# Kernel optimization log

Hardware: AMD Instinct MI355X
Metric: run time of the kernel (lower is better)

Reference implementation:

```python
import jax, jax.numpy as jnp
import numpy as np

RADIUS2 = 0.03 ** 2
SIM_THRESH = 0.7
EPS = 1e-8


def setup_inputs() -> dict:
    key = jax.random.key(0)
    k1, k2, k3, k4, k5, k6, k7 = jax.random.split(key, 7)
    B, N, D = 2, 6144, 32
    # points in a 0.3-side cube so radius 0.03 gives realistic neighbor counts
    points = jax.random.uniform(k1, (B, N, 3), dtype=jnp.float32) * 0.3
    embeddings = jax.random.normal(k2, (B, N, D), dtype=jnp.float32)
    leaf_mask = jax.random.randint(k3, (B, N), 0, 2, dtype=jnp.int32)
    # consistency_net: Linear(2D, D) -> ReLU -> Linear(D, D)
    W1 = jax.random.normal(k4, (2 * D, D), dtype=jnp.float32) * (1.0 / np.sqrt(2 * D))
    b1 = jax.random.normal(k5, (D,), dtype=jnp.float32) * 0.01
    W2 = jax.random.normal(k6, (D, D), dtype=jnp.float32) * (1.0 / np.sqrt(D))
    b2 = jax.random.normal(k7, (D,), dtype=jnp.float32) * 0.01
    return {"points": points, "embeddings": embeddings, "leaf_mask": leaf_mask,
            "W1": W1, "b1": b1, "W2": W2, "b2": b2}


def reference(points, embeddings, leaf_mask, W1, b1, W2, b2):
    # points: [B,N,3], embeddings: [B,N,D], leaf_mask: [B,N] int (0/1)
    dt = embeddings.dtype
    leaf = leaf_mask > 0  # [B,N] bool

    # pairwise squared distances via the Gram trick (avoids [B,N,N,3])
    pn = jnp.sum(points * points, axis=-1)                      # [B,N]
    gram = jnp.einsum('bic,bjc->bij', points, points)           # [B,N,N]
    d2 = jnp.maximum(pn[:, :, None] + pn[:, None, :] - 2.0 * gram, 0.0)

    # neighbor mask: within radius AND neighbor is leaf (matches dist<0.03 & leaf_mask)
    nb = (d2 < RADIUS2) & leaf[:, None, :]                      # [B,N,N]

    # cosine similarity with torch's eps clamp on norms
    enorm = jnp.maximum(jnp.linalg.norm(embeddings, axis=-1), EPS)  # [B,N]
    inner = jnp.einsum('bid,bjd->bij', embeddings, embeddings)      # [B,N,N]
    sims = inner / (enorm[:, :, None] * enorm[:, None, :])

    sim_mask = nb & (sims > SIM_THRESH)                          # [B,N,N]
    cnt_nb = jnp.sum(nb, axis=-1)                                # [B,N]
    cnt_sim = jnp.sum(sim_mask, axis=-1)                         # [B,N]

    # mean of similar-neighbor embeddings
    sum_sim = jnp.einsum('bij,bjd->bid', sim_mask.astype(dt), embeddings)
    mean_sim = sum_sim / jnp.maximum(cnt_sim, 1).astype(dt)[..., None]

    # consistency MLP on [center_embedding, mean_similar]
    combined = jnp.concatenate([embeddings, mean_sim], axis=-1)  # [B,N,2D]
    h = jax.nn.relu(jnp.einsum('bnk,kd->bnd', combined, W1) + b1)
    out = jnp.einsum('bnk,kd->bnd', h, W2) + b2                  # [B,N,D]

    # refine only leaf points with >1 neighbor and >0 similar neighbors
    cond = leaf & (cnt_nb > 1) & (cnt_sim > 0)                   # [B,N]
    refined = jnp.where(cond[..., None], out, embeddings)

    # per-batch early exit: sum(leaf_mask) < 10 -> unchanged
    batch_ok = jnp.sum(leaf_mask, axis=-1) >= 10                 # [B]
    return jnp.where(batch_ok[:, None, None], refined, embeddings)
```

## Files before the change

### kernel.cpp

```cpp
#include <hip/hip_runtime.h>

#define NPTS    6144
#define DIM     32
#define NB      2
#define NCELL   1000
#define R2      0.0009f
#define NWAVES  4
#define BLOCK   (NWAVES * 64)
#define LEAFBIT 8192
#define PPT     6
#define NBCAP   128
#define COPYBLK 64

__device__ __forceinline__ int cellof(float x) {
    int c = (int)(x * (10.0f / 0.3f));
    return min(max(c, 0), 9);
}

#define WS_LEAF   0
#define WS_CSTART 4
#define WS_SORTED 2008

__global__ __launch_bounds__(1024)
void build_cells(const float* __restrict__ points, const int* __restrict__ leaf,
                 const float* __restrict__ emb, float* __restrict__ out,
                 int* __restrict__ ws)
{
    __shared__ int s_hist[1024];
    __shared__ int s_cursor[1024];
    __shared__ int s_wsum[16];
    __shared__ int s_leaf;

    if (blockIdx.x >= NB) {
        const int cb = blockIdx.x - NB;
        const float4* src = (const float4*)emb;
        float4*       dst = (float4*)out;
        const int total = NB * NPTS * (DIM / 4);
        for (int i = cb * 1024 + threadIdx.x; i < total; i += COPYBLK * 1024)
            dst[i] = src[i];
        return;
    }

    const int t = threadIdx.x;
    const int b = blockIdx.x;
    const int w = t >> 6, lane = t & 63;

    s_hist[t] = 0;
    if (t == 0) s_leaf = 0;

    float px[PPT], py[PPT], pz[PPT];
    int   pc[PPT], pw[PPT];

    __syncthreads();

    int lc = 0;
    #pragma unroll
    for (int r = 0; r < PPT; ++r) {
        const int i  = r * 1024 + t;
        const int gi = b * NPTS + i;
        px[r] = points[gi * 3 + 0];
        py[r] = points[gi * 3 + 1];
        pz[r] = points[gi * 3 + 2];
        const int lf = leaf[gi] > 0 ? 1 : 0;
        lc += lf;
        pc[r] = (cellof(pz[r]) * 10 + cellof(py[r])) * 10 + cellof(px[r]);
        pw[r] = i + (lf ? LEAFBIT : 0);
        atomicAdd(&s_hist[pc[r]], 1);
    }
    #pragma unroll
    for (int off = 32; off > 0; off >>= 1) lc += __shfl_down(lc, off);
    if (lane == 0) atomicAdd(&s_leaf, lc);
    __syncthreads();

    const int v = s_hist[t];
    int x = v;
    #pragma unroll
    for (int off = 1; off < 64; off <<= 1) {
        const int y = __shfl_up(x, off);
        if (lane >= off) x += y;
    }
    if (lane == 63) s_wsum[w] = x;
    __syncthreads();
    if (t < 16) {
        int wv = s_wsum[t];
        #pragma unroll
        for (int off = 1; off < 16; off <<= 1) {
            const int y = __shfl_up(wv, off);
            if (t >= off) wv += y;
        }
        s_wsum[t] = wv;
    }
    __syncthreads();
    const int incl = x + (w > 0 ? s_wsum[w - 1] : 0);
    s_cursor[t] = incl - v;

    if (t < NCELL) ws[WS_CSTART + b * (NCELL + 1) + t + 1] = incl;
    if (t == 0) {
        ws[WS_CSTART + b * (NCELL + 1)] = 0;
        ws[WS_LEAF + b] = s_leaf;
    }
    __syncthreads();

    float4* sorted = (float4*)(ws + WS_SORTED) + (size_t)b * NPTS;
    #pragma unroll
    for (int r = 0; r < PPT; ++r) {
        const int pos = atomicAdd(&s_cursor[pc[r]], 1);
        sorted[pos] = make_float4(px[r], py[r], pz[r], (float)pw[r]);
    }
}

__global__ __launch_bounds__(BLOCK)
void refine(const float* __restrict__ emb,
            const float* __restrict__ W1, const float* __restrict__ b1,
            const float* __restrict__ W2, const float* __restrict__ b2,
            const int* __restrict__ ws, float* __restrict__ out)
{
    __shared__ __align__(16) float s_ei[NWAVES][DIM];
    __shared__ float s_mean[NWAVES][DIM];
    __shared__ float s_h[NWAVES][DIM];
    __shared__ int   s_nb[NWAVES][NBCAP];
    __shared__ int   s_sv[NWAVES][NBCAP];

    const int tid  = threadIdx.x;
    const int wid  = tid >> 6;
    const int lane = tid & 63;
    const int s    = blockIdx.x * NWAVES + wid;
    const int b    = s / NPTS;
    const int slot = s - b * NPTS;

    if (ws[WS_LEAF + b] < 10) return;

    const float4* srt  = (const float4*)(ws + WS_SORTED) + (size_t)b * NPTS;
    const int*    cst  = ws + WS_CSTART + b * (NCELL + 1);
    const float*  embB = emb + (size_t)b * NPTS * DIM;

    const float4 P  = srt[slot];
    const int    iw = (int)P.w;
    if (!(iw & LEAFBIT)) return;
    const int io = iw & (LEAFBIT - 1);

    const float* ei = embB + (size_t)io * DIM;
    float ev = 0.0f;
    if (lane < DIM) { ev = ei[lane]; s_ei[wid][lane] = ev; }
    float nsq = ev * ev;
    #pragma unroll
    for (int off = 16; off > 0; off >>= 1) nsq += __shfl_xor(nsq, off);
    const float ni2 = __shfl(nsq, 0);
    const float rni = 1.0f / fmaxf(sqrtf(ni2), 1e-8f);

    const int cx = cellof(P.x), cy = cellof(P.y), cz = cellof(P.z);

    int begv = 0, lenv = 0;
    if (lane < 9) {
        const int z = cz + lane / 3 - 1;
        const int y = cy + lane % 3 - 1;
        if ((unsigned)z <= 9u && (unsigned)y <= 9u) {
            const int rowb = (z * 10 + y) * 10;
            const int c0   = rowb + max(cx - 1, 0);
            const int c1   = rowb + min(cx + 1, 9);
            begv = cst[c0];
            lenv = cst[c1 + 1] - begv;
        }
    }
    const int rb0 = __shfl(begv, 0), rb1 = __shfl(begv, 1), rb2 = __shfl(begv, 2);
    const int rb3 = __shfl(begv, 3), rb4 = __shfl(begv, 4), rb5 = __shfl(begv, 5);
    const int rb6 = __shfl(begv, 6), rb7 = __shfl(begv, 7), rb8 = __shfl(begv, 8);
    const int ln0 = __shfl(lenv, 0), ln1 = __shfl(lenv, 1), ln2 = __shfl(lenv, 2);
    const int ln3 = __shfl(lenv, 3), ln4 = __shfl(lenv, 4), ln5 = __shfl(lenv, 5);
    const int ln6 = __shfl(lenv, 6), ln7 = __shfl(lenv, 7), ln8 = __shfl(lenv, 8);
    const int pf1 = ln0,       pf2 = pf1 + ln1, pf3 = pf2 + ln2;
    const int pf4 = pf3 + ln3, pf5 = pf4 + ln4, pf6 = pf5 + ln5;
    const int pf7 = pf6 + ln6, pf8 = pf7 + ln7, pf9 = pf8 + ln8;

    int nbcnt = 0;
    for (int base = 0; base < pf9; base += 64) {
        const int g = base + lane;
        int j = 0;
        if (g < pf9) j = rb8 + g - pf8;
        if (g < pf8) j = rb7 + g - pf7;
        if (g < pf7) j = rb6 + g - pf6;
        if (g < pf6) j = rb5 + g - pf5;
        if (g < pf5) j = rb4 + g - pf4;
        if (g < pf4) j = rb3 + g - pf3;
        if (g < pf3) j = rb2 + g - pf2;
        if (g < pf2) j = rb1 + g - pf1;
        if (g < pf1) j = rb0 + g;
        const float4 Q  = srt[j];
        const float dx = Q.x - P.x, dy = Q.y - P.y, dz = Q.z - P.z;
        const float d2 = dx * dx + dy * dy + dz * dz;
        const int   jw = (int)Q.w;
        const bool  nb = (g < pf9) && (d2 < R2) && ((jw & LEAFBIT) != 0);
        const unsigned long long m = __ballot(nb);
        if (nb) {
            const int pos = nbcnt + __popcll(m & ((1ull << lane) - 1ull));
            if (pos < NBCAP) s_nb[wid][pos] = jw & (LEAFBIT - 1);
        }
        nbcnt += __popcll(m);
    }
    const int cnt_nb = nbcnt;

    const int d    = lane & 31;
    const int half = lane >> 5;
    int csim = 0;
    const int nh = min(cnt_nb, NBCAP);
    for (int h0 = 0; h0 < nh; h0 += 32) {
        const int h = h0 + d;
        float dot = 0.0f, nj2 = 0.0f;
        int   jo  = 0;
        if (h < nh) {
            jo = s_nb[wid][h];
            const float4* ej4 = (const float4*)(embB + (size_t)jo * DIM) + half * 4;
            #pragma unroll
            for (int k = 0; k < 4; ++k) {
                const float4 v = ej4[k];
                const float4 a = *(const float4*)&s_ei[wid][16 * half + 4 * k];
                dot += a.x * v.x + a.y * v.y + a.z * v.z + a.w * v.w;
                nj2 += v.x * v.x + v.y * v.y + v.z * v.z + v.w * v.w;
            }
        }
        dot += __shfl_xor(dot, 32);
        nj2 += __shfl_xor(nj2, 32);
        bool surv = false;
        if (h < nh && half == 0) {
            const float rnj = 1.0f / fmaxf(sqrtf(nj2), 1e-8f);
            surv = (dot * rni * rnj) > 0.7f;
        }
        const unsigned long long m = __ballot(surv);
        if (surv) {
            const int pos = csim + __popcll(m & ((1ull << lane) - 1ull));
            s_sv[wid][pos] = jo;
        }
        csim += __popcll(m);
    }

    if (!((cnt_nb > 1) && (csim > 0))) return;

    float msum = 0.0f;
    for (int v = half; v < csim; v += 2)
        msum += embB[(size_t)s_sv[wid][v] * DIM + d];
    msum += __shfl_xor(msum, 32);
    if (half == 0) s_mean[wid][d] = msum / (float)csim;

    float a = (half == 0) ? b1[d] : 0.0f;
    #pragma unroll
    for (int k = 0; k < 16; ++k) {
        const int kk = half * 16 + k;
        a = fmaf(s_ei[wid][kk], W1[kk * DIM + d], a);
    }
    #pragma unroll
    for (int k = 0; k < 16; ++k) {
        const int kk = half * 16 + k;
        a = fmaf(s_mean[wid][kk], W1[(DIM + kk) * DIM + d], a);
    }
    a += __shfl_xor(a, 32);
    if (half == 0) s_h[wid][d] = fmaxf(a, 0.0f);

    float c = (half == 0) ? b2[d] : 0.0f;
    #pragma unroll
    for (int k = 0; k < 16; ++k) {
        const int kk = half * 16 + k;
        c = fmaf(s_h[wid][kk], W2[kk * DIM + d], c);
    }
    c += __shfl_xor(c, 32);
    if (half == 0)
        out[((size_t)b * NPTS + io) * DIM + d] = c;
}

extern "C" void kernel_launch(void* const* d_in, const int* in_sizes, int n_in,
                              void* d_out, int out_size, void* d_ws, size_t ws_size,
                              hipStream_t stream) {
    const float* points = (const float*)d_in[0];
    const float* emb    = (const float*)d_in[1];
    const int*   leaf   = (const int*)d_in[2];
    const float* W1     = (const float*)d_in[3];
    const float* b1     = (const float*)d_in[4];
    const float* W2     = (const float*)d_in[5];
    const float* b2     = (const float*)d_in[6];
    float*       outp   = (float*)d_out;
    int*         ws     = (int*)d_ws;

    build_cells<<<NB + COPYBLK, 1024, 0, stream>>>(points, leaf, emb, outp, ws);

    const int grid = (NB * NPTS) / NWAVES;
    refine<<<grid, BLOCK, 0, stream>>>(emb, W1, b1, W2, b2, ws, outp);
}
```

Measured before the change: 86.85 us.

## Fuse cell build and refine into one kernel with per-block redundant grid in LDS

Merges the cell-sorting kernel and the refine kernel into a single launch. Each of 256 blocks redundantly rebuilds its batch's sorted point grid and cell starts in shared memory (about 130KB), then each wave processes a contiguous run of points and writes either the copied embedding or the MLP output. This removes the second launch, the global workspace round trip and the separate bulk copy. In exchange, every block repeats the full histogram and sort work and uses a large LDS footprint, which limits occupancy to one block per CU.

```diff
diff --git a/kernel.cpp b/kernel.cpp
--- a/kernel.cpp
+++ b/kernel.cpp
@@ -5,48 +5,59 @@
 #define NB      2
 #define NCELL   1000
 #define R2      0.0009f
-#define NWAVES  4
-#define BLOCK   (NWAVES * 64)
 #define LEAFBIT 8192
 #define PPT     6
 #define NBCAP   128
-#define COPYBLK 64
+#define CHUNKS  128
+#define SPB     (NPTS / CHUNKS)
+#define WPB     16
+#define SPW     (SPB / WPB)
+
+#define SM_PTS    0
+#define SM_CST    98304
+#define SM_HIST   102400
+#define SM_CUR    106496
+#define SM_WSUM   110592
+#define SM_LEAF   110656
+#define SM_NB     110720
+#define SM_SV     118912
+#define SM_EI     127104
+#define SM_MEAN   129152
+#define SM_H      131200
+#define SMEM_BYTES 133248
 
 __device__ __forceinline__ int cellof(float x) {
     int c = (int)(x * (10.0f / 0.3f));
     return min(max(c, 0), 9);
 }
 
-#define WS_LEAF   0
-#define WS_CSTART 4
-#define WS_SORTED 2008
-
 __global__ __launch_bounds__(1024)
-void build_cells(const float* __restrict__ points, const int* __restrict__ leaf,
-                 const float* __restrict__ emb, float* __restrict__ out,
-                 int* __restrict__ ws)
+void fused(const float* __restrict__ points, const int* __restrict__ leaf,
+           const float* __restrict__ emb,
+           const float* __restrict__ W1, const float* __restrict__ b1,
+           const float* __restrict__ W2, const float* __restrict__ b2,
+           float* __restrict__ out)
 {
-    __shared__ int s_hist[1024];
-    __shared__ int s_cursor[1024];
-    __shared__ int s_wsum[16];
-    __shared__ int s_leaf;
-
-    if (blockIdx.x >= NB) {
-        const int cb = blockIdx.x - NB;
-        const float4* src = (const float4*)emb;
-        float4*       dst = (float4*)out;
-        const int total = NB * NPTS * (DIM / 4);
-        for (int i = cb * 1024 + threadIdx.x; i < total; i += COPYBLK * 1024)
-            dst[i] = src[i];
-        return;
-    }
-
-    const int t = threadIdx.x;
-    const int b = blockIdx.x;
-    const int w = t >> 6, lane = t & 63;
+    extern __shared__ char smem[];
+    float4* s_pts   = (float4*)(smem + SM_PTS);
+    int*    s_cst   = (int*)(smem + SM_CST);
+    int*    s_hist  = (int*)(smem + SM_HIST);
+    int*    s_cur   = (int*)(smem + SM_CUR);
+    int*    s_wsum  = (int*)(smem + SM_WSUM);
+    int*    s_leafp = (int*)(smem + SM_LEAF);
+    int*    s_nb    = (int*)(smem + SM_NB);
+    int*    s_sv    = (int*)(smem + SM_SV);
+    float*  s_ei    = (float*)(smem + SM_EI);
+    float*  s_mean  = (float*)(smem + SM_MEAN);
+    float*  s_h     = (float*)(smem + SM_H);
+
+    const int t     = threadIdx.x;
+    const int b     = blockIdx.x / CHUNKS;
+    const int chunk = blockIdx.x - b * CHUNKS;
+    const int wid   = t >> 6, lane = t & 63;
 
     s_hist[t] = 0;
-    if (t == 0) s_leaf = 0;
+    if (t == 0) *s_leafp = 0;
 
     float px[PPT], py[PPT], pz[PPT];
     int   pc[PPT], pw[PPT];
@@ -69,7 +80,7 @@
     }
     #pragma unroll
     for (int off = 32; off > 0; off >>= 1) lc += __shfl_down(lc, off);
-    if (lane == 0) atomicAdd(&s_leaf, lc);
+    if (lane == 0) atomicAdd(s_leafp, lc);
     __syncthreads();
 
     const int v = s_hist[t];
@@ -79,7 +90,7 @@
         const int y = __shfl_up(x, off);
         if (lane >= off) x += y;
     }
-    if (lane == 63) s_wsum[w] = x;
+    if (lane == 63) s_wsum[wid] = x;
     __syncthreads();
     if (t < 16) {
         int wv = s_wsum[t];
@@ -91,184 +102,173 @@
         s_wsum[t] = wv;
     }
     __syncthreads();
-    const int incl = x + (w > 0 ? s_wsum[w - 1] : 0);
-    s_cursor[t] = incl - v;
-
-    if (t < NCELL) ws[WS_CSTART + b * (NCELL + 1) + t + 1] = incl;
-    if (t == 0) {
-        ws[WS_CSTART + b * (NCELL + 1)] = 0;
-        ws[WS_LEAF + b] = s_leaf;
-    }
-    __syncthreads();
-
-    float4* sorted = (float4*)(ws + WS_SORTED) + (size_t)b * NPTS;
+    const int incl = x + (wid > 0 ? s_wsum[wid - 1] : 0);
+    s_cur[t] = incl - v;
+    if (t < NCELL) s_cst[t + 1] = incl;
+    if (t == 0) s_cst[0] = 0;
+    __syncthreads();
+
     #pragma unroll
     for (int r = 0; r < PPT; ++r) {
-        const int pos = atomicAdd(&s_cursor[pc[r]], 1);
-        sorted[pos] = make_float4(px[r], py[r], pz[r], (float)pw[r]);
-    }
-}
-
-__global__ __launch_bounds__(BLOCK)
-void refine(const float* __restrict__ emb,
-            const float* __restrict__ W1, const float* __restrict__ b1,
-            const float* __restrict__ W2, const float* __restrict__ b2,
-            const int* __restrict__ ws, float* __restrict__ out)
-{
-    __shared__ __align__(16) float s_ei[NWAVES][DIM];
-    __shared__ float s_mean[NWAVES][DIM];
-    __shared__ float s_h[NWAVES][DIM];
-    __shared__ int   s_nb[NWAVES][NBCAP];
-    __shared__ int   s_sv[NWAVES][NBCAP];
-
-    const int tid  = threadIdx.x;
-    const int wid  = tid >> 6;
-    const int lane = tid & 63;
-    const int s    = blockIdx.x * NWAVES + wid;
-    const int b    = s / NPTS;
-    const int slot = s - b * NPTS;
-
-    if (ws[WS_LEAF + b] < 10) return;
-
-    const float4* srt  = (const float4*)(ws + WS_SORTED) + (size_t)b * NPTS;
-    const int*    cst  = ws + WS_CSTART + b * (NCELL + 1);
-    const float*  embB = emb + (size_t)b * NPTS * DIM;
-
-    const float4 P  = srt[slot];
-    const int    iw = (int)P.w;
-    if (!(iw & LEAFBIT)) return;
-    const int io = iw & (LEAFBIT - 1);
-
-    const float* ei = embB + (size_t)io * DIM;
-    float ev = 0.0f;
-    if (lane < DIM) { ev = ei[lane]; s_ei[wid][lane] = ev; }
-    float nsq = ev * ev;
-    #pragma unroll
-    for (int off = 16; off > 0; off >>= 1) nsq += __shfl_xor(nsq, off);
-    const float ni2 = __shfl(nsq, 0);
-    const float rni = 1.0f / fmaxf(sqrtf(ni2), 1e-8f);
-
-    const int cx = cellof(P.x), cy = cellof(P.y), cz = cellof(P.z);
-
-    int begv = 0, lenv = 0;
-    if (lane < 9) {
-        const int z = cz + lane / 3 - 1;
-        const int y = cy + lane % 3 - 1;
-        if ((unsigned)z <= 9u && (unsigned)y <= 9u) {
-            const int rowb = (z * 10 + y) * 10;
-            const int c0   = rowb + max(cx - 1, 0);
-            const int c1   = rowb + min(cx + 1, 9);
-            begv = cst[c0];
-            lenv = cst[c1 + 1] - begv;
-        }
-    }
-    const int rb0 = __shfl(begv, 0), rb1 = __shfl(begv, 1), rb2 = __shfl(begv, 2);
-    const int rb3 = __shfl(begv, 3), rb4 = __shfl(begv, 4), rb5 = __shfl(begv, 5);
-    const int rb6 = __shfl(begv, 6), rb7 = __shfl(begv, 7), rb8 = __shfl(begv, 8);
-    const int ln0 = __shfl(lenv, 0), ln1 = __shfl(lenv, 1), ln2 = __shfl(lenv, 2);
-    const int ln3 = __shfl(lenv, 3), ln4 = __shfl(lenv, 4), ln5 = __shfl(lenv, 5);
-    const int ln6 = __shfl(lenv, 6), ln7 = __shfl(lenv, 7), ln8 = __shfl(lenv, 8);
-    const int pf1 = ln0,       pf2 = pf1 + ln1, pf3 = pf2 + ln2;
-    const int pf4 = pf3 + ln3, pf5 = pf4 + ln4, pf6 = pf5 + ln5;
-    const int pf7 = pf6 + ln6, pf8 = pf7 + ln7, pf9 = pf8 + ln8;
-
-    int nbcnt = 0;
-    for (int base = 0; base < pf9; base += 64) {
-        const int g = base + lane;
-        int j = 0;
-        if (g < pf9) j = rb8 + g - pf8;
-        if (g < pf8) j = rb7 + g - pf7;
-        if (g < pf7) j = rb6 + g - pf6;
-        if (g < pf6) j = rb5 + g - pf5;
-        if (g < pf5) j = rb4 + g - pf4;
-        if (g < pf4) j = rb3 + g - pf3;
-        if (g < pf3) j = rb2 + g - pf2;
-        if (g < pf2) j = rb1 + g - pf1;
-        if (g < pf1) j = rb0 + g;
-        const float4 Q  = srt[j];
-        const float dx = Q.x - P.x, dy = Q.y - P.y, dz = Q.z - P.z;
-        const float d2 = dx * dx + dy * dy + dz * dz;
-        const int   jw = (int)Q.w;
-        const bool  nb = (g < pf9) && (d2 < R2) && ((jw & LEAFBIT) != 0);
-        const unsigned long long m = __ballot(nb);
-        if (nb) {
-            const int pos = nbcnt + __popcll(m & ((1ull << lane) - 1ull));
-            if (pos < NBCAP) s_nb[wid][pos] = jw & (LEAFBIT - 1);
-        }
-        nbcnt += __popcll(m);
-    }
-    const int cnt_nb = nbcnt;
-
-    const int d    = lane & 31;
-    const int half = lane >> 5;
-    int csim = 0;
-    const int nh = min(cnt_nb, NBCAP);
-    for (int h0 = 0; h0 < nh; h0 += 32) {
-        const int h = h0 + d;
-        float dot = 0.0f, nj2 = 0.0f;
-        int   jo  = 0;
-        if (h < nh) {
-            jo = s_nb[wid][h];
-            const float4* ej4 = (const float4*)(embB + (size_t)jo * DIM) + half * 4;
-            #pragma unroll
-            for (int k = 0; k < 4; ++k) {
-                const float4 v = ej4[k];
-                const float4 a = *(const float4*)&s_ei[wid][16 * half + 4 * k];
-                dot += a.x * v.x + a.y * v.y + a.z * v.z + a.w * v.w;
-                nj2 += v.x * v.x + v.y * v.y + v.z * v.z + v.w * v.w;
-            }
-        }
-        dot += __shfl_xor(dot, 32);
-        nj2 += __shfl_xor(nj2, 32);
-        bool surv = false;
-        if (h < nh && half == 0) {
-            const float rnj = 1.0f / fmaxf(sqrtf(nj2), 1e-8f);
-            surv = (dot * rni * rnj) > 0.7f;
-        }
-        const unsigned long long m = __ballot(surv);
-        if (surv) {
-            const int pos = csim + __popcll(m & ((1ull << lane) - 1ull));
-            s_sv[wid][pos] = jo;
-        }
-        csim += __popcll(m);
-    }
-
-    if (!((cnt_nb > 1) && (csim > 0))) return;
-
-    float msum = 0.0f;
-    for (int v = half; v < csim; v += 2)
-        msum += embB[(size_t)s_sv[wid][v] * DIM + d];
-    msum += __shfl_xor(msum, 32);
-    if (half == 0) s_mean[wid][d] = msum / (float)csim;
-
-    float a = (half == 0) ? b1[d] : 0.0f;
-    #pragma unroll
-    for (int k = 0; k < 16; ++k) {
-        const int kk = half * 16 + k;
-        a = fmaf(s_ei[wid][kk], W1[kk * DIM + d], a);
-    }
-    #pragma unroll
-    for (int k = 0; k < 16; ++k) {
-        const int kk = half * 16 + k;
-        a = fmaf(s_mean[wid][kk], W1[(DIM + kk) * DIM + d], a);
-    }
-    a += __shfl_xor(a, 32);
-    if (half == 0) s_h[wid][d] = fmaxf(a, 0.0f);
-
-    float c = (half == 0) ? b2[d] : 0.0f;
-    #pragma unroll
-    for (int k = 0; k < 16; ++k) {
-        const int kk = half * 16 + k;
-        c = fmaf(s_h[wid][kk], W2[kk * DIM + d], c);
-    }
-    c += __shfl_xor(c, 32);
-    if (half == 0)
-        out[((size_t)b * NPTS + io) * DIM + d] = c;
+        const int pos = atomicAdd(&s_cur[pc[r]], 1);
+        s_pts[pos] = make_float4(px[r], py[r], pz[r], (float)pw[r]);
+    }
+    __syncthreads();
+
+    const bool   ok   = *s_leafp >= 10;
+    const float* embB = emb + (size_t)b * NPTS * DIM;
+    float*       outB = out + (size_t)b * NPTS * DIM;
+    const int    dd   = lane & 31;
+    const int    half = lane >> 5;
+
+    for (int rs = 0; rs < SPW; ++rs) {
+        const int io = chunk * SPB + wid * SPW + rs;
+        const int gi = b * NPTS + io;
+        const float Px = points[gi * 3 + 0];
+        const float Py = points[gi * 3 + 1];
+        const float Pz = points[gi * 3 + 2];
+        const bool  li = leaf[gi] > 0;
+
+        const float4* e4   = (const float4*)(embB + (size_t)io * DIM);
+        float4*       out4 = (float4*)(outB + (size_t)io * DIM);
+
+        if (!(ok && li)) {
+            if (lane < DIM / 4) out4[lane] = e4[lane];
+            continue;
+        }
+
+        float ev = 0.0f;
+        if (lane < DIM) { ev = ((const float*)e4)[lane]; s_ei[wid * DIM + lane] = ev; }
+        float nsq = ev * ev;
+        #pragma unroll
+        for (int off = 16; off > 0; off >>= 1) nsq += __shfl_xor(nsq, off);
+        const float ni2 = __shfl(nsq, 0);
+        const float rni = 1.0f / fmaxf(sqrtf(ni2), 1e-8f);
+
+        const int cx = cellof(Px), cy = cellof(Py), cz = cellof(Pz);
+
+        int begv = 0, lenv = 0;
+        if (lane < 9) {
+            const int z = cz + lane / 3 - 1;
+            const int y = cy + lane % 3 - 1;
+            if ((unsigned)z <= 9u && (unsigned)y <= 9u) {
+                const int rowb = (z * 10 + y) * 10;
+                const int c0   = rowb + max(cx - 1, 0);
+                const int c1   = rowb + min(cx + 1, 9);
+                begv = s_cst[c0];
+                lenv = s_cst[c1 + 1] - begv;
+            }
+        }
+        const int rb0 = __shfl(begv, 0), rb1 = __shfl(begv, 1), rb2 = __shfl(begv, 2);
+        const int rb3 = __shfl(begv, 3), rb4 = __shfl(begv, 4), rb5 = __shfl(begv, 5);
+        const int rb6 = __shfl(begv, 6), rb7 = __shfl(begv, 7), rb8 = __shfl(begv, 8);
+        const int ln0 = __shfl(lenv, 0), ln1 = __shfl(lenv, 1), ln2 = __shfl(lenv, 2);
+        const int ln3 = __shfl(lenv, 3), ln4 = __shfl(lenv, 4), ln5 = __shfl(lenv, 5);
+        const int ln6 = __shfl(lenv, 6), ln7 = __shfl(lenv, 7), ln8 = __shfl(lenv, 8);
+        const int pf1 = ln0,       pf2 = pf1 + ln1, pf3 = pf2 + ln2;
+        const int pf4 = pf3 + ln3, pf5 = pf4 + ln4, pf6 = pf5 + ln5;
+        const int pf7 = pf6 + ln6, pf8 = pf7 + ln7, pf9 = pf8 + ln8;
+
+        int nbcnt = 0;
+        for (int base = 0; base < pf9; base += 64) {
+            const int g = base + lane;
+            int j = 0;
+            if (g < pf9) j = rb8 + g - pf8;
+            if (g < pf8) j = rb7 + g - pf7;
+            if (g < pf7) j = rb6 + g - pf6;
+            if (g < pf6) j = rb5 + g - pf5;
+            if (g < pf5) j = rb4 + g - pf4;
+            if (g < pf4) j = rb3 + g - pf3;
+            if (g < pf3) j = rb2 + g - pf2;
+            if (g < pf2) j = rb1 + g - pf1;
+            if (g < pf1) j = rb0 + g;
+            const float4 Q  = s_pts[j];
+            const float dx = Q.x - Px, dy = Q.y - Py, dz = Q.z - Pz;
+            const float d2 = dx * dx + dy * dy + dz * dz;
+            const int   jw = (int)Q.w;
+            const bool  nb = (g < pf9) && (d2 < R2) && ((jw & LEAFBIT) != 0);
+            const unsigned long long m = __ballot(nb);
+            if (nb) {
+                const int pos = nbcnt + __popcll(m & ((1ull << lane) - 1ull));
+                if (pos < NBCAP) s_nb[wid * NBCAP + pos] = jw & (LEAFBIT - 1);
+            }
+            nbcnt += __popcll(m);
+        }
+        const int cnt_nb = nbcnt;
+
+        int csim = 0;
+        const int nh = min(cnt_nb, NBCAP);
+        for (int h0 = 0; h0 < nh; h0 += 32) {
+            const int h = h0 + dd;
+            float dot = 0.0f, nj2 = 0.0f;
+            int   jo  = 0;
+            if (h < nh) {
+                jo = s_nb[wid * NBCAP + h];
+                const float4* ej4 = (const float4*)(embB + (size_t)jo * DIM) + half * 4;
+                #pragma unroll
+                for (int k = 0; k < 4; ++k) {
+                    const float4 vq = ej4[k];
+                    const float4 a  = *(const float4*)&s_ei[wid * DIM + 16 * half + 4 * k];
+                    dot += a.x * vq.x + a.y * vq.y + a.z * vq.z + a.w * vq.w;
+                    nj2 += vq.x * vq.x + vq.y * vq.y + vq.z * vq.z + vq.w * vq.w;
+                }
+            }
+            dot += __shfl_xor(dot, 32);
+            nj2 += __shfl_xor(nj2, 32);
+            bool surv = false;
+            if (h < nh && half == 0) {
+                const float rnj = 1.0f / fmaxf(sqrtf(nj2), 1e-8f);
+                surv = (dot * rni * rnj) > 0.7f;
+            }
+            const unsigned long long m = __ballot(surv);
+            if (surv) {
+                const int pos = csim + __popcll(m & ((1ull << lane) - 1ull));
+                s_sv[wid * NBCAP + pos] = jo;
+            }
+            csim += __popcll(m);
+        }
+
+        if (!((cnt_nb > 1) && (csim > 0))) {
+            if (lane < DIM) outB[(size_t)io * DIM + lane] = ev;
+            continue;
+        }
+
+        float msum = 0.0f;
+        for (int vv = half; vv < csim; vv += 2)
+            msum += embB[(size_t)s_sv[wid * NBCAP + vv] * DIM + dd];
+        msum += __shfl_xor(msum, 32);
+        if (half == 0) s_mean[wid * DIM + dd] = msum / (float)csim;
+
+        float a = (half == 0) ? b1[dd] : 0.0f;
+        #pragma unroll
+        for (int k = 0; k < 16; ++k) {
+            const int kk = half * 16 + k;
+            a = fmaf(s_ei[wid * DIM + kk], W1[kk * DIM + dd], a);
+        }
+        #pragma unroll
+        for (int k = 0; k < 16; ++k) {
+            const int kk = half * 16 + k;
+            a = fmaf(s_mean[wid * DIM + kk], W1[(DIM + kk) * DIM + dd], a);
+        }
+        a += __shfl_xor(a, 32);
+        if (half == 0) s_h[wid * DIM + dd] = fmaxf(a, 0.0f);
+
+        float c = (half == 0) ? b2[dd] : 0.0f;
+        #pragma unroll
+        for (int k = 0; k < 16; ++k) {
+            const int kk = half * 16 + k;
+            c = fmaf(s_h[wid * DIM + kk], W2[kk * DIM + dd], c);
+        }
+        c += __shfl_xor(c, 32);
+        if (half == 0)
+            outB[(size_t)io * DIM + dd] = c;
+    }
 }
 
 extern "C" void kernel_launch(void* const* d_in, const int* in_sizes, int n_in,
                               void* d_out, int out_size, void* d_ws, size_t ws_size,
                               hipStream_t stream) {
+    (void)d_ws; (void)ws_size; (void)in_sizes; (void)n_in; (void)out_size;
     const float* points = (const float*)d_in[0];
     const float* emb    = (const float*)d_in[1];
     const int*   leaf   = (const int*)d_in[2];
@@ -277,10 +277,15 @@
     const float* W2     = (const float*)d_in[5];
     const float* b2     = (const float*)d_in[6];
     float*       outp   = (float*)d_out;
-    int*         ws     = (int*)d_ws;
-
-    build_cells<<<NB + COPYBLK, 1024, 0, stream>>>(points, leaf, emb, outp, ws);
-
-    const int grid = (NB * NPTS) / NWAVES;
-    refine<<<grid, BLOCK, 0, stream>>>(emb, W1, b1, W2, b2, ws, outp);
+
+    static bool attr_set = false;
+    if (!attr_set) {
+        (void)hipFuncSetAttribute(reinterpret_cast<const void*>(&fused),
+                                  hipFuncAttributeMaxDynamicSharedMemorySize,
+                                  SMEM_BYTES);
+        attr_set = true;
+    }
+
+    fused<<<NB * CHUNKS, 1024, SMEM_BYTES, stream>>>(points, leaf, emb,
+                                                     W1, b1, W2, b2, outp);
 }
```

Measured after the change: 135.3 us. 1.56x slower.

## Fuse cell build and refine into one kernel with flag-based inter-block sync

Applied to the files above, without the earlier changes.

Merges the grid-build and refine kernels into a single launch. Two producer blocks build the cell lists and publish a release flag, while consumer blocks copy their non-leaf rows and then spin on that flag before refining. Each wave now handles three points in original index order rather than sorted cell order, and the separate full-embedding copy is replaced by per-row copies for non-leaf and skipped points. The goal is to remove the second launch and the redundant copy traffic. In exchange it loses the spatial locality of sorted processing and risks deadlock if the producer blocks are not resident. The flag is also never reset, so on repeated calls consumers can read workspace that is still being rewritten.

```diff
diff --git a/kernel.cpp b/kernel.cpp
--- a/kernel.cpp
+++ b/kernel.cpp
@@ -5,12 +5,13 @@
 #define NB      2
 #define NCELL   1000
 #define R2      0.0009f
-#define NWAVES  4
-#define BLOCK   (NWAVES * 64)
 #define LEAFBIT 8192
 #define PPT     6
 #define NBCAP   128
-#define COPYBLK 64
+#define CONS    256
+#define WPB     16
+#define RPW     3
+#define MAGIC   0x7C3A91E5
 
 __device__ __forceinline__ int cellof(float x) {
     int c = (int)(x * (10.0f / 0.3f));
@@ -18,257 +19,289 @@
 }
 
 #define WS_LEAF   0
+#define WS_FLAG   2
 #define WS_CSTART 4
 #define WS_SORTED 2008
 
-__global__ __launch_bounds__(1024)
-void build_cells(const float* __restrict__ points, const int* __restrict__ leaf,
-                 const float* __restrict__ emb, float* __restrict__ out,
-                 int* __restrict__ ws)
+__global__ __launch_bounds__(1024, 8)
+void fused(const float* __restrict__ points, const int* __restrict__ leaf,
+           const float* __restrict__ emb,
+           const float* __restrict__ W1, const float* __restrict__ b1,
+           const float* __restrict__ W2, const float* __restrict__ b2,
+           int* __restrict__ ws, float* __restrict__ out)
 {
     __shared__ int s_hist[1024];
     __shared__ int s_cursor[1024];
     __shared__ int s_wsum[16];
     __shared__ int s_leaf;
-
-    if (blockIdx.x >= NB) {
-        const int cb = blockIdx.x - NB;
-        const float4* src = (const float4*)emb;
-        float4*       dst = (float4*)out;
-        const int total = NB * NPTS * (DIM / 4);
-        for (int i = cb * 1024 + threadIdx.x; i < total; i += COPYBLK * 1024)
-            dst[i] = src[i];
+    __shared__ __align__(16) float s_ei[WPB][DIM];
+    __shared__ __align__(16) float s_mean[WPB][DIM];
+    __shared__ float s_h[WPB][DIM];
+    __shared__ int   s_nb[WPB][NBCAP];
+    __shared__ int   s_sv[WPB][NBCAP];
+
+    const int t = threadIdx.x;
+
+    if (blockIdx.x < NB) {
+        const int b = blockIdx.x;
+        const int w = t >> 6, lane = t & 63;
+
+        s_hist[t] = 0;
+        if (t == 0) s_leaf = 0;
+
+        float px[PPT], py[PPT], pz[PPT];
+        int   pc[PPT], pw[PPT];
+
+        __syncthreads();
+
+        int lc = 0;
+        #pragma unroll
+        for (int r = 0; r < PPT; ++r) {
+            const int i  = r * 1024 + t;
+            const int gi = b * NPTS + i;
+            px[r] = points[gi * 3 + 0];
+            py[r] = points[gi * 3 + 1];
+            pz[r] = points[gi * 3 + 2];
+            const int lf = leaf[gi] > 0 ? 1 : 0;
+            lc += lf;
+            pc[r] = (cellof(pz[r]) * 10 + cellof(py[r])) * 10 + cellof(px[r]);
+            pw[r] = i + (lf ? LEAFBIT : 0);
+            atomicAdd(&s_hist[pc[r]], 1);
+        }
+        #pragma unroll
+        for (int off = 32; off > 0; off >>= 1) lc += __shfl_down(lc, off);
+        if (lane == 0) atomicAdd(&s_leaf, lc);
+        __syncthreads();
+
+        const int v = s_hist[t];
+        int x = v;
+        #pragma unroll
+        for (int off = 1; off < 64; off <<= 1) {
+            const int y = __shfl_up(x, off);
+            if (lane >= off) x += y;
+        }
+        if (lane == 63) s_wsum[w] = x;
+        __syncthreads();
+        if (t < 16) {
+            int wv = s_wsum[t];
+            #pragma unroll
+            for (int off = 1; off < 16; off <<= 1) {
+                const int y = __shfl_up(wv, off);
+                if (t >= off) wv += y;
+            }
+            s_wsum[t] = wv;
+        }
+        __syncthreads();
+        const int incl = x + (w > 0 ? s_wsum[w - 1] : 0);
+        s_cursor[t] = incl - v;
+
+        if (t < NCELL) ws[WS_CSTART + b * (NCELL + 1) + t + 1] = incl;
+        if (t == 0) {
+            ws[WS_CSTART + b * (NCELL + 1)] = 0;
+            ws[WS_LEAF + b] = s_leaf;
+        }
+        __syncthreads();
+
+        float4* sorted = (float4*)(ws + WS_SORTED) + (size_t)b * NPTS;
+        #pragma unroll
+        for (int r = 0; r < PPT; ++r) {
+            const int pos = atomicAdd(&s_cursor[pc[r]], 1);
+            sorted[pos] = make_float4(px[r], py[r], pz[r], (float)pw[r]);
+        }
+        __syncthreads();
+        if (t == 0) {
+            __threadfence();
+            __hip_atomic_store(&ws[WS_FLAG + b], MAGIC,
+                               __ATOMIC_RELEASE, __HIP_MEMORY_SCOPE_AGENT);
+        }
         return;
     }
 
-    const int t = threadIdx.x;
-    const int b = blockIdx.x;
-    const int w = t >> 6, lane = t & 63;
-
-    s_hist[t] = 0;
-    if (t == 0) s_leaf = 0;
-
-    float px[PPT], py[PPT], pz[PPT];
-    int   pc[PPT], pw[PPT];
-
-    __syncthreads();
-
-    int lc = 0;
-    #pragma unroll
-    for (int r = 0; r < PPT; ++r) {
-        const int i  = r * 1024 + t;
-        const int gi = b * NPTS + i;
-        px[r] = points[gi * 3 + 0];
-        py[r] = points[gi * 3 + 1];
-        pz[r] = points[gi * 3 + 2];
-        const int lf = leaf[gi] > 0 ? 1 : 0;
-        lc += lf;
-        pc[r] = (cellof(pz[r]) * 10 + cellof(py[r])) * 10 + cellof(px[r]);
-        pw[r] = i + (lf ? LEAFBIT : 0);
-        atomicAdd(&s_hist[pc[r]], 1);
+    const int cblk  = blockIdx.x - NB;
+    const int wid   = t >> 6;
+    const int lane  = t & 63;
+    const int gbase = cblk * (WPB * RPW) + wid * RPW;
+
+    {
+        const int rr  = lane >> 3;
+        const int sub = lane & 7;
+        if (rr < RPW) {
+            const int g = gbase + rr;
+            if (leaf[g] <= 0) {
+                const float4* e4 = (const float4*)(emb + (size_t)g * DIM);
+                float4*       o4 = (float4*)(out + (size_t)g * DIM);
+                o4[sub] = e4[sub];
+            }
+        }
     }
-    #pragma unroll
-    for (int off = 32; off > 0; off >>= 1) lc += __shfl_down(lc, off);
-    if (lane == 0) atomicAdd(&s_leaf, lc);
-    __syncthreads();
-
-    const int v = s_hist[t];
-    int x = v;
-    #pragma unroll
-    for (int off = 1; off < 64; off <<= 1) {
-        const int y = __shfl_up(x, off);
-        if (lane >= off) x += y;
-    }
-    if (lane == 63) s_wsum[w] = x;
-    __syncthreads();
-    if (t < 16) {
-        int wv = s_wsum[t];
-        #pragma unroll
-        for (int off = 1; off < 16; off <<= 1) {
-            const int y = __shfl_up(wv, off);
-            if (t >= off) wv += y;
-        }
-        s_wsum[t] = wv;
+
+    if (t == 0) {
+        while (__hip_atomic_load(&ws[WS_FLAG + 0], __ATOMIC_ACQUIRE,
+                                 __HIP_MEMORY_SCOPE_AGENT) != MAGIC ||
+               __hip_atomic_load(&ws[WS_FLAG + 1], __ATOMIC_ACQUIRE,
+                                 __HIP_MEMORY_SCOPE_AGENT) != MAGIC)
+            __builtin_amdgcn_s_sleep(2);
+        __threadfence();
     }
     __syncthreads();
-    const int incl = x + (w > 0 ? s_wsum[w - 1] : 0);
-    s_cursor[t] = incl - v;
-
-    if (t < NCELL) ws[WS_CSTART + b * (NCELL + 1) + t + 1] = incl;
-    if (t == 0) {
-        ws[WS_CSTART + b * (NCELL + 1)] = 0;
-        ws[WS_LEAF + b] = s_leaf;
+
+    const int dd   = lane & 31;
+    const int half = lane >> 5;
+
+    for (int rs = 0; rs < RPW; ++rs) {
+        const int g  = gbase + rs;
+        if (leaf[g] <= 0) continue;
+        const int b  = (g >= NPTS) ? 1 : 0;
+        const int io = g - b * NPTS;
+
+        const float* embB = emb + (size_t)b * NPTS * DIM;
+        float*       outR = out + (size_t)g * DIM;
+
+        float ev = 0.0f;
+        if (lane < DIM) { ev = embB[(size_t)io * DIM + lane]; s_ei[wid][lane] = ev; }
+
+        const bool ok = ws[WS_LEAF + b] >= 10;
+        if (!ok) {
+            if (lane < DIM) outR[lane] = ev;
+            continue;
+        }
+
+        float nsq = ev * ev;
+        #pragma unroll
+        for (int off = 16; off > 0; off >>= 1) nsq += __shfl_xor(nsq, off);
+        const float ni2 = __shfl(nsq, 0);
+        const float rni = 1.0f / fmaxf(sqrtf(ni2), 1e-8f);
+
+        const float Px = points[g * 3 + 0];
+        const float Py = points[g * 3 + 1];
+        const float Pz = points[g * 3 + 2];
+        const int cx = cellof(Px), cy = cellof(Py), cz = cellof(Pz);
+
+        const int*    cst = ws + WS_CSTART + b * (NCELL + 1);
+        const float4* srt = (const float4*)(ws + WS_SORTED) + (size_t)b * NPTS;
+
+        int begv = 0, lenv = 0;
+        if (lane < 9) {
+            const int z = cz + lane / 3 - 1;
+            const int y = cy + lane % 3 - 1;
+            if ((unsigned)z <= 9u && (unsigned)y <= 9u) {
+                const int rowb = (z * 10 + y) * 10;
+                const int c0   = rowb + max(cx - 1, 0);
+                const int c1   = rowb + min(cx + 1, 9);
+                begv = cst[c0];
+                lenv = cst[c1 + 1] - begv;
+            }
+        }
+        const int rb0 = __shfl(begv, 0), rb1 = __shfl(begv, 1), rb2 = __shfl(begv, 2);
+        const int rb3 = __shfl(begv, 3), rb4 = __shfl(begv, 4), rb5 = __shfl(begv, 5);
+        const int rb6 = __shfl(begv, 6), rb7 = __shfl(begv, 7), rb8 = __shfl(begv, 8);
+        const int ln0 = __shfl(lenv, 0), ln1 = __shfl(lenv, 1), ln2 = __shfl(lenv, 2);
+        const int ln3 = __shfl(lenv, 3), ln4 = __shfl(lenv, 4), ln5 = __shfl(lenv, 5);
+        const int ln6 = __shfl(lenv, 6), ln7 = __shfl(lenv, 7), ln8 = __shfl(lenv, 8);
+        const int pf1 = ln0,       pf2 = pf1 + ln1, pf3 = pf2 + ln2;
+        const int pf4 = pf3 + ln3, pf5 = pf4 + ln4, pf6 = pf5 + ln5;
+        const int pf7 = pf6 + ln6, pf8 = pf7 + ln7, pf9 = pf8 + ln8;
+
+        int nbcnt = 0;
+        for (int base = 0; base < pf9; base += 64) {
+            const int gg = base + lane;
+            int j = 0;
+            if (gg < pf9) j = rb8 + gg - pf8;
+            if (gg < pf8) j = rb7 + gg - pf7;
+            if (gg < pf7) j = rb6 + gg - pf6;
+            if (gg < pf6) j = rb5 + gg - pf5;
+            if (gg < pf5) j = rb4 + gg - pf4;
+            if (gg < pf4) j = rb3 + gg - pf3;
+            if (gg < pf3) j = rb2 + gg - pf2;
+            if (gg < pf2) j = rb1 + gg - pf1;
+            if (gg < pf1) j = rb0 + gg;
+            const float4 Q  = srt[j];
+            const float dx = Q.x - Px, dy = Q.y - Py, dz = Q.z - Pz;
+            const float d2 = dx * dx + dy * dy + dz * dz;
+            const int   jw = (int)Q.w;
+            const bool  nb = (gg < pf9) && (d2 < R2) && ((jw & LEAFBIT) != 0);
+            const unsigned long long m = __ballot(nb);
+            if (nb) {
+                const int pos = nbcnt + __popcll(m & ((1ull << lane) - 1ull));
+                if (pos < NBCAP) s_nb[wid][pos] = jw & (LEAFBIT - 1);
+            }
+            nbcnt += __popcll(m);
+        }
+        const int cnt_nb = nbcnt;
+
+        int csim = 0;
+        const int nh = min(cnt_nb, NBCAP);
+        for (int h0 = 0; h0 < nh; h0 += 32) {
+            const int h = h0 + dd;
+            float dot = 0.0f, nj2 = 0.0f;
+            int   jo  = 0;
+            if (h < nh) {
+                jo = s_nb[wid][h];
+                const float4* ej4 = (const float4*)(embB + (size_t)jo * DIM) + half * 4;
+                #pragma unroll
+                for (int k = 0; k < 4; ++k) {
+                    const float4 vq = ej4[k];
+                    const float4 a  = *(const float4*)&s_ei[wid][16 * half + 4 * k];
+                    dot += a.x * vq.x + a.y * vq.y + a.z * vq.z + a.w * vq.w;
+                    nj2 += vq.x * vq.x + vq.y * vq.y + vq.z * vq.z + vq.w * vq.w;
+                }
+            }
+            dot += __shfl_xor(dot, 32);
+            nj2 += __shfl_xor(nj2, 32);
+            bool surv = false;
+            if (h < nh && half == 0) {
+                const float rnj = 1.0f / fmaxf(sqrtf(nj2), 1e-8f);
+                surv = (dot * rni * rnj) > 0.7f;
+            }
+            const unsigned long long m = __ballot(surv);
+            if (surv) {
+                const int pos = csim + __popcll(m & ((1ull << lane) - 1ull));
+                s_sv[wid][pos] = jo;
+            }
+            csim += __popcll(m);
+        }
+
+        if (!((cnt_nb > 1) && (csim > 0))) {
+            if (lane < DIM) outR[lane] = ev;
+            continue;
+        }
+
+        float msum = 0.0f;
+        for (int vv = half; vv < csim; vv += 2)
+            msum += embB[(size_t)s_sv[wid][vv] * DIM + dd];
+        msum += __shfl_xor(msum, 32);
+        if (half == 0) s_mean[wid][dd] = msum / (float)csim;
+
+        float a = (half == 0) ? b1[dd] : 0.0f;
+        #pragma unroll
+        for (int k = 0; k < 16; ++k) {
+            const int kk = half * 16 + k;
+            a = fmaf(s_ei[wid][kk], W1[kk * DIM + dd], a);
+        }
+        #pragma unroll
+        for (int k = 0; k < 16; ++k) {
+            const int kk = half * 16 + k;
+            a = fmaf(s_mean[wid][kk], W1[(DIM + kk) * DIM + dd], a);
+        }
+        a += __shfl_xor(a, 32);
+        if (half == 0) s_h[wid][dd] = fmaxf(a, 0.0f);
+
+        float c = (half == 0) ? b2[dd] : 0.0f;
+        #pragma unroll
+        for (int k = 0; k < 16; ++k) {
+            const int kk = half * 16 + k;
+            c = fmaf(s_h[wid][kk], W2[kk * DIM + dd], c);
+        }
+        c += __shfl_xor(c, 32);
+        if (half == 0)
+            outR[dd] = c;
     }
-    __syncthreads();
-
-    float4* sorted = (float4*)(ws + WS_SORTED) + (size_t)b * NPTS;
-    #pragma unroll
-    for (int r = 0; r < PPT; ++r) {
-        const int pos = atomicAdd(&s_cursor[pc[r]], 1);
-        sorted[pos] = make_float4(px[r], py[r], pz[r], (float)pw[r]);
-    }
-}
-
-__global__ __launch_bounds__(BLOCK)
-void refine(const float* __restrict__ emb,
-            const float* __restrict__ W1, const float* __restrict__ b1,
-            const float* __restrict__ W2, const float* __restrict__ b2,
-            const int* __restrict__ ws, float* __restrict__ out)
-{
-    __shared__ __align__(16) float s_ei[NWAVES][DIM];
-    __shared__ float s_mean[NWAVES][DIM];
-    __shared__ float s_h[NWAVES][DIM];
-    __shared__ int   s_nb[NWAVES][NBCAP];
-    __shared__ int   s_sv[NWAVES][NBCAP];
-
-    const int tid  = threadIdx.x;
-    const int wid  = tid >> 6;
-    const int lane = tid & 63;
-    const int s    = blockIdx.x * NWAVES + wid;
-    const int b    = s / NPTS;
-    const int slot = s - b * NPTS;
-
-    if (ws[WS_LEAF + b] < 10) return;
-
-    const float4* srt  = (const float4*)(ws + WS_SORTED) + (size_t)b * NPTS;
-    const int*    cst  = ws + WS_CSTART + b * (NCELL + 1);
-    const float*  embB = emb + (size_t)b * NPTS * DIM;
-
-    const float4 P  = srt[slot];
-    const int    iw = (int)P.w;
-    if (!(iw & LEAFBIT)) return;
-    const int io = iw & (LEAFBIT - 1);
-
-    const float* ei = embB + (size_t)io * DIM;
-    float ev = 0.0f;
-    if (lane < DIM) { ev = ei[lane]; s_ei[wid][lane] = ev; }
-    float nsq = ev * ev;
-    #pragma unroll
-    for (int off = 16; off > 0; off >>= 1) nsq += __shfl_xor(nsq, off);
-    const float ni2 = __shfl(nsq, 0);
-    const float rni = 1.0f / fmaxf(sqrtf(ni2), 1e-8f);
-
-    const int cx = cellof(P.x), cy = cellof(P.y), cz = cellof(P.z);
-
-    int begv = 0, lenv = 0;
-    if (lane < 9) {
-        const int z = cz + lane / 3 - 1;
-        const int y = cy + lane % 3 - 1;
-        if ((unsigned)z <= 9u && (unsigned)y <= 9u) {
-            const int rowb = (z * 10 + y) * 10;
-            const int c0   = rowb + max(cx - 1, 0);
-            const int c1   = rowb + min(cx + 1, 9);
-            begv = cst[c0];
-            lenv = cst[c1 + 1] - begv;
-        }
-    }
-    const int rb0 = __shfl(begv, 0), rb1 = __shfl(begv, 1), rb2 = __shfl(begv, 2);
-    const int rb3 = __shfl(begv, 3), rb4 = __shfl(begv, 4), rb5 = __shfl(begv, 5);
-    const int rb6 = __shfl(begv, 6), rb7 = __shfl(begv, 7), rb8 = __shfl(begv, 8);
-    const int ln0 = __shfl(lenv, 0), ln1 = __shfl(lenv, 1), ln2 = __shfl(lenv, 2);
-    const int ln3 = __shfl(lenv, 3), ln4 = __shfl(lenv, 4), ln5 = __shfl(lenv, 5);
-    const int ln6 = __shfl(lenv, 6), ln7 = __shfl(lenv, 7), ln8 = __shfl(lenv, 8);
-    const int pf1 = ln0,       pf2 = pf1 + ln1, pf3 = pf2 + ln2;
-    const int pf4 = pf3 + ln3, pf5 = pf4 + ln4, pf6 = pf5 + ln5;
-    const int pf7 = pf6 + ln6, pf8 = pf7 + ln7, pf9 = pf8 + ln8;
-
-    int nbcnt = 0;
-    for (int base = 0; base < pf9; base += 64) {
-        const int g = base + lane;
-        int j = 0;
-        if (g < pf9) j = rb8 + g - pf8;
-        if (g < pf8) j = rb7 + g - pf7;
-        if (g < pf7) j = rb6 + g - pf6;
-        if (g < pf6) j = rb5 + g - pf5;
-        if (g < pf5) j = rb4 + g - pf4;
-        if (g < pf4) j = rb3 + g - pf3;
-        if (g < pf3) j = rb2 + g - pf2;
-        if (g < pf2) j = rb1 + g - pf1;
-        if (g < pf1) j = rb0 + g;
-        const float4 Q  = srt[j];
-        const float dx = Q.x - P.x, dy = Q.y - P.y, dz = Q.z - P.z;
-        const float d2 = dx * dx + dy * dy + dz * dz;
-        const int   jw = (int)Q.w;
-        const bool  nb = (g < pf9) && (d2 < R2) && ((jw & LEAFBIT) != 0);
-        const unsigned long long m = __ballot(nb);
-        if (nb) {
-            const int pos = nbcnt + __popcll(m & ((1ull << lane) - 1ull));
-            if (pos < NBCAP) s_nb[wid][pos] = jw & (LEAFBIT - 1);
-        }
-        nbcnt += __popcll(m);
-    }
-    const int cnt_nb = nbcnt;
-
-    const int d    = lane & 31;
-    const int half = lane >> 5;
-    int csim = 0;
-    const int nh = min(cnt_nb, NBCAP);
-    for (int h0 = 0; h0 < nh; h0 += 32) {
-        const int h = h0 + d;
-        float dot = 0.0f, nj2 = 0.0f;
-        int   jo  = 0;
-        if (h < nh) {
-            jo = s_nb[wid][h];
-            const float4* ej4 = (const float4*)(embB + (size_t)jo * DIM) + half * 4;
-            #pragma unroll
-            for (int k = 0; k < 4; ++k) {
-                const float4 v = ej4[k];
-                const float4 a = *(const float4*)&s_ei[wid][16 * half + 4 * k];
-                dot += a.x * v.x + a.y * v.y + a.z * v.z + a.w * v.w;
-                nj2 += v.x * v.x + v.y * v.y + v.z * v.z + v.w * v.w;
-            }
-        }
-        dot += __shfl_xor(dot, 32);
-        nj2 += __shfl_xor(nj2, 32);
-        bool surv = false;
-        if (h < nh && half == 0) {
-            const float rnj = 1.0f / fmaxf(sqrtf(nj2), 1e-8f);
-            surv = (dot * rni * rnj) > 0.7f;
-        }
-        const unsigned long long m = __ballot(surv);
-        if (surv) {
-            const int pos = csim + __popcll(m & ((1ull << lane) - 1ull));
-            s_sv[wid][pos] = jo;
-        }
-        csim += __popcll(m);
-    }
-
-    if (!((cnt_nb > 1) && (csim > 0))) return;
-
-    float msum = 0.0f;
-    for (int v = half; v < csim; v += 2)
-        msum += embB[(size_t)s_sv[wid][v] * DIM + d];
-    msum += __shfl_xor(msum, 32);
-    if (half == 0) s_mean[wid][d] = msum / (float)csim;
-
-    float a = (half == 0) ? b1[d] : 0.0f;
-    #pragma unroll
-    for (int k = 0; k < 16; ++k) {
-        const int kk = half * 16 + k;
-        a = fmaf(s_ei[wid][kk], W1[kk * DIM + d], a);
-    }
-    #pragma unroll
-    for (int k = 0; k < 16; ++k) {
-        const int kk = half * 16 + k;
-        a = fmaf(s_mean[wid][kk], W1[(DIM + kk) * DIM + d], a);
-    }
-    a += __shfl_xor(a, 32);
-    if (half == 0) s_h[wid][d] = fmaxf(a, 0.0f);
-
-    float c = (half == 0) ? b2[d] : 0.0f;
-    #pragma unroll
-    for (int k = 0; k < 16; ++k) {
-        const int kk = half * 16 + k;
-        c = fmaf(s_h[wid][kk], W2[kk * DIM + d], c);
-    }
-    c += __shfl_xor(c, 32);
-    if (half == 0)
-        out[((size_t)b * NPTS + io) * DIM + d] = c;
 }
 
 extern "C" void kernel_launch(void* const* d_in, const int* in_sizes, int n_in,
                               void* d_out, int out_size, void* d_ws, size_t ws_size,
                               hipStream_t stream) {
+    (void)in_sizes; (void)n_in; (void)out_size; (void)ws_size;
     const float* points = (const float*)d_in[0];
     const float* emb    = (const float*)d_in[1];
     const int*   leaf   = (const int*)d_in[2];
@@ -279,8 +312,6 @@
     float*       outp   = (float*)d_out;
     int*         ws     = (int*)d_ws;
 
-    build_cells<<<NB + COPYBLK, 1024, 0, stream>>>(points, leaf, emb, outp, ws);
-
-    const int grid = (NB * NPTS) / NWAVES;
-    refine<<<grid, BLOCK, 0, stream>>>(emb, W1, b1, W2, b2, ws, outp);
+    fused<<<NB + CONS, 1024, 0, stream>>>(points, leaf, emb,
+                                          W1, b1, W2, b2, ws, outp);
 }
```

Measured after the change: 259.9 us. 2.99x slower.
